# Optimization experiments

Hardware: AMD Instinct MI355X
Metric: run time of the kernel (lower is better)

The kernel has to match this reference:

```python
import jax, jax.numpy as jnp
import numpy as np
from jax import lax

WINDOW_SIZE = 11
SIGMA = 1.5
MAX_VAL = 1.0
C1 = (MAX_VAL * 0.01) ** 2
C2 = (MAX_VAL * 0.03) ** 2


def _make_window(channel: int, k: int = WINDOW_SIZE, sigma: float = SIGMA) -> np.ndarray:
    x = np.arange(k, dtype=np.float64)
    g = np.exp(-((x - k // 2) ** 2) / (2.0 * sigma ** 2))
    g = (g / g.sum()).astype(np.float32)
    # rank-1 separable 3D window, built as dense [C,1,k,k,k] kernel (OIDHW, groups=C)
    w3 = g[:, None, None] * g[None, :, None] * g[None, None, :]
    return np.broadcast_to(w3, (channel, 1, k, k, k)).copy()


def _dwconv3d(x, kernel, pad):
    # depthwise 3D conv, SAME padding for odd kernel
    return lax.conv_general_dilated(
        x, kernel, window_strides=(1, 1, 1), padding=[(pad, pad)] * 3,
        dimension_numbers=("NCDHW", "OIDHW", "NCDHW"),
        feature_group_count=kernel.shape[0])


def setup_inputs() -> dict:
    key = jax.random.key(0)
    k1, k2 = jax.random.split(key)
    shape = (2, 4, 64, 160, 160)  # [B, C, D, H, W]
    img1 = jax.random.uniform(k1, shape, dtype=jnp.float32)
    img2 = jax.random.uniform(k2, shape, dtype=jnp.float32)
    return {"img1": img1, "img2": img2}


def reference(img1, img2):
    channel = img1.shape[1]
    window = jnp.asarray(_make_window(channel))
    pad = WINDOW_SIZE // 2
    # mask = ones_like(img1) in the original -> identity multiply, omitted
    mu1 = _dwconv3d(img1, window, pad)
    mu2 = _dwconv3d(img2, window, pad)
    mu1_sq = mu1 * mu1
    mu2_sq = mu2 * mu2
    mu1_mu2 = mu1 * mu2
    sigma1_sq = _dwconv3d(img1 * img1, window, pad) - mu1_sq
    sigma2_sq = _dwconv3d(img2 * img2, window, pad) - mu2_sq
    sigma12 = _dwconv3d(img1 * img2, window, pad) - mu1_mu2
    ssim_map = ((2.0 * mu1_mu2 + C1) * (2.0 * sigma12 + C2)) / (
        (mu1_sq + mu2_sq + C1) * (sigma1_sq + sigma2_sq + C2))
    ssim = jnp.mean(ssim_map, axis=(0, 2, 3, 4))  # per-channel SSIM, shape [C]
    return 1.0 - ssim
```

## Files before the change

### kernel.cpp

```cpp
#include <hip/hip_runtime.h>
#include <math.h>

typedef float v2f __attribute__((ext_vector_type(2)));

namespace {

constexpr int C_DIM = 4;
constexpr int D_DIM = 64;
constexpr int H_DIM = 160;
constexpr int W_DIM = 160;

constexpr int TH = 20;
constexpr int TW = 20;
constexpr int HALO = 5;
constexpr int EH = 30;
constexpr int EW = 30;
constexpr int XST = 31;
constexpr int MST = 21;
constexpr int NPIX = EH * EW;

constexpr int TILES_W = 8;
constexpr int TPC = 64;
constexpr int D_SPLIT = 2;
constexpr int DCH = D_DIM / D_SPLIT;
constexpr int NBLOCKS = D_SPLIT * 2 * C_DIM * TPC;

constexpr float C1f = 1e-4f;
constexpr float C2f = 9e-4f;
constexpr float INV_N = 1.0f / (2.0f * 64.0f * 160.0f * 160.0f);

struct GW { float g[11]; };

}

__global__ void finalize_kernel(const float* __restrict__ partial,
                                float* __restrict__ out) {
    const int tid = threadIdx.x;
    const int c = tid >> 6;
    const int lane = tid & 63;
    float s = 0.0f;
#pragma unroll
    for (int r = 0; r < D_SPLIT * 2; ++r)
        s += partial[(r * C_DIM + c) * TPC + lane];
#pragma unroll
    for (int off = 32; off > 0; off >>= 1) s += __shfl_down(s, off, 64);
    if (lane == 0 && c < C_DIM) out[c] = 1.0f - s * INV_N;
}

__global__ __launch_bounds__(256, 2) void ssim3d_kernel(
    const float* __restrict__ img1, const float* __restrict__ img2,
    float* __restrict__ partial, GW gwp) {

    const int bid = blockIdx.x;
    const int tile = bid % TPC;
    const int c = (bid / TPC) % C_DIM;
    const int rest = bid / (TPC * C_DIM);
    const int b = rest & 1;
    const int dh = rest >> 1;
    const int h0 = (tile / TILES_W) * TH;
    const int w0 = (tile % TILES_W) * TW;

    const int d_lo = dh * DCH;
    const int s_base = (d_lo == 0) ? 0 : ((d_lo - HALO) & ~3);
    const int s_hi = min(D_DIM - 1, d_lo + DCH - 1 + HALO);
    const bool has_tail = (d_lo + DCH == D_DIM);

    const long planeHW = (long)H_DIM * W_DIM;
    const long volbase = (long)(b * C_DIM + c) * D_DIM * planeHW;
    const long org = volbase + (long)(h0 - HALO) * W_DIM + (w0 - HALO);
    const float* __restrict__ p1 = img1 + org;
    const float* __restrict__ p2 = img2 + org;

    const bool interior = (h0 >= HALO) && (h0 + TH + HALO <= H_DIM) &&
                          (w0 >= HALO) && (w0 + TW + HALO <= W_DIM);

    __shared__ v2f    xy[2][EH][XST];
    __shared__ float4 mid[2][EH][MST];
    __shared__ float  rbuf[4];

    const int tid = threadIdx.x;

    int hh_[4], ww_[4], off_[4];
    bool live_[4], ok_[4];
#pragma unroll
    for (int k = 0; k < 4; ++k) {
        const int e = tid + k * 256;
        live_[k] = (e < NPIX);
        const int hh = e / EW;
        const int ww = e - hh * EW;
        hh_[k] = hh; ww_[k] = ww;
        off_[k] = hh * W_DIM + ww;
        const int gh = h0 - HALO + hh;
        const int gw = w0 - HALO + ww;
        ok_[k] = ((unsigned)gh < (unsigned)H_DIM) &&
                 ((unsigned)gw < (unsigned)W_DIM);
    }

    auto fetch_slice = [&](int s, v2f lv[4]) {
        const long sb = (long)s * planeHW;
#pragma unroll
        for (int k = 0; k < 4; ++k) {
            lv[k] = (v2f){0.0f, 0.0f};
            if (live_[k] && (interior || ok_[k])) {
                const long gi = sb + off_[k];
                lv[k].x = p1[gi];
                lv[k].y = p2[gi];
            }
        }
    };
    auto commit_slice = [&](int buf, const v2f lv[4]) {
#pragma unroll
        for (int k = 0; k < 4; ++k)
            if (live_[k]) xy[buf][hh_[k]][ww_[k]] = lv[k];
    };

    const bool wactive = (tid < 150);
    const int whh = tid % 30;
    const int wg  = (tid / 30) * 4;

    auto wconv = [&](int cur) {
        v2f a0 = {0.f,0.f}, a1 = {0.f,0.f}, a2 = {0.f,0.f}, a3 = {0.f,0.f};
        v2f q0 = {0.f,0.f}, q1 = {0.f,0.f}, q2 = {0.f,0.f}, q3 = {0.f,0.f};
#pragma unroll
        for (int t = 0; t < 14; ++t) {
            const v2f xv = xy[cur][whh][wg + t];
            v2f qp;
            qp.x = fmaf(xv.x, xv.x, xv.y * xv.y);
            qp.y = xv.x * xv.y;
            if (t <= 10) {
                const v2f g2 = {gwp.g[t], gwp.g[t]};
                a0 = __builtin_elementwise_fma(g2, xv, a0);
                q0 = __builtin_elementwise_fma(g2, qp, q0);
            }
            if (t >= 1 && t <= 11) {
                const v2f g2 = {gwp.g[t-1], gwp.g[t-1]};
                a1 = __builtin_elementwise_fma(g2, xv, a1);
                q1 = __builtin_elementwise_fma(g2, qp, q1);
            }
            if (t >= 2 && t <= 12) {
                const v2f g2 = {gwp.g[t-2], gwp.g[t-2]};
                a2 = __builtin_elementwise_fma(g2, xv, a2);
                q2 = __builtin_elementwise_fma(g2, qp, q2);
            }
            if (t >= 3) {
                const v2f g2 = {gwp.g[t-3], gwp.g[t-3]};
                a3 = __builtin_elementwise_fma(g2, xv, a3);
                q3 = __builtin_elementwise_fma(g2, qp, q3);
            }
        }
        mid[cur][whh][wg]     = make_float4(a0.x, a0.y, q0.x, q0.y);
        mid[cur][whh][wg + 1] = make_float4(a1.x, a1.y, q1.x, q1.y);
        mid[cur][whh][wg + 2] = make_float4(a2.x, a2.y, q2.x, q2.y);
        mid[cur][whh][wg + 3] = make_float4(a3.x, a3.y, q3.x, q3.y);
    };

    const bool hworker = (tid < 200);
    const int hw = tid % 20;
    const int hb = (tid / 20) * 2;

    float accum = 0.0f;
    auto ssim_add = [&](v2f mxy, v2f mqp) {
        const float m1 = mxy.x, m2 = mxy.y;
        const float q = mqp.x, pp = mqp.y;
        const float m1s = m1 * m1;
        const float m2s = m2 * m2;
        const float m12 = m1 * m2;
        const float spp = q - m1s - m2s;
        const float s12 = pp - m12;
        const float num = (2.0f * m12 + C1f) * (2.0f * s12 + C2f);
        const float den = (m1s + m2s + C1f) * (spp + C2f);
        accum = fmaf(num, __builtin_amdgcn_rcpf(den), accum);
    };

    v2f w0xy[14], w0qp[14], w1xy[14], w1qp[14];
#pragma unroll
    for (int i = 0; i < 14; ++i) {
        w0xy[i] = (v2f){0.f, 0.f}; w0qp[i] = (v2f){0.f, 0.f};
        w1xy[i] = (v2f){0.f, 0.f}; w1qp[i] = (v2f){0.f, 0.f};
    }

    {
        v2f lv[4];
        fetch_slice(s_base, lv);
        commit_slice(0, lv);
    }
    __syncthreads();

    for (int sb = s_base; sb <= s_hi; sb += 4) {
#pragma unroll
        for (int u = 0; u < 4; ++u) {
            const int s = sb + u;
            if (s > s_hi) break;
            v2f lv[4];
            const bool have_next = (s + 1 <= s_hi);
            if (have_next) fetch_slice(s + 1, lv);
            if (wactive) wconv(u & 1);
            if (have_next) commit_slice((u + 1) & 1, lv);
            __syncthreads();
            if (hworker) {
                v2f z0x = {0.f,0.f}, z0q = {0.f,0.f};
                v2f z1x = {0.f,0.f}, z1q = {0.f,0.f};
#pragma unroll
                for (int t = 0; t < 12; ++t) {
                    const float4 m = mid[u & 1][hb + t][hw];
                    const v2f ma = {m.x, m.y};
                    const v2f mb = {m.z, m.w};
                    if (t <= 10) {
                        const v2f g2 = {gwp.g[t], gwp.g[t]};
                        z0x = __builtin_elementwise_fma(g2, ma, z0x);
                        z0q = __builtin_elementwise_fma(g2, mb, z0q);
                    }
                    if (t >= 1) {
                        const v2f g2 = {gwp.g[t-1], gwp.g[t-1]};
                        z1x = __builtin_elementwise_fma(g2, ma, z1x);
                        z1q = __builtin_elementwise_fma(g2, mb, z1q);
                    }
                }
                w0xy[10 + u] = z0x; w0qp[10 + u] = z0q;
                w1xy[10 + u] = z1x; w1qp[10 + u] = z1q;
                if (s >= d_lo + HALO) {
                    v2f mx0 = {0.f,0.f}, mq0 = {0.f,0.f};
                    v2f mx1 = {0.f,0.f}, mq1 = {0.f,0.f};
#pragma unroll
                    for (int t = 0; t < 11; ++t) {
                        const v2f g2 = {gwp.g[t], gwp.g[t]};
                        mx0 = __builtin_elementwise_fma(g2, w0xy[u + t], mx0);
                        mq0 = __builtin_elementwise_fma(g2, w0qp[u + t], mq0);
                        mx1 = __builtin_elementwise_fma(g2, w1xy[u + t], mx1);
                        mq1 = __builtin_elementwise_fma(g2, w1qp[u + t], mq1);
                    }
                    ssim_add(mx0, mq0);
                    ssim_add(mx1, mq1);
                }
            }
        }
        if (hworker) {
#pragma unroll
            for (int k = 0; k < 10; ++k) {
                w0xy[k] = w0xy[k + 4]; w0qp[k] = w0qp[k + 4];
                w1xy[k] = w1xy[k + 4]; w1qp[k] = w1qp[k + 4];
            }
        }
    }

    if (has_tail && hworker) {
#pragma unroll
        for (int i = 10; i < 14; ++i) {
            w0xy[i] = (v2f){0.f, 0.f}; w0qp[i] = (v2f){0.f, 0.f};
            w1xy[i] = (v2f){0.f, 0.f}; w1qp[i] = (v2f){0.f, 0.f};
        }
#pragma unroll
        for (int u2 = 0; u2 < 5; ++u2) {
            v2f mx0 = {0.f,0.f}, mq0 = {0.f,0.f};
            v2f mx1 = {0.f,0.f}, mq1 = {0.f,0.f};
#pragma unroll
            for (int t = 0; t < 11; ++t) {
                if (u2 + t <= 13) {
                    const v2f g2 = {gwp.g[t], gwp.g[t]};
                    mx0 = __builtin_elementwise_fma(g2, w0xy[u2 + t], mx0);
                    mq0 = __builtin_elementwise_fma(g2, w0qp[u2 + t], mq0);
                    mx1 = __builtin_elementwise_fma(g2, w1xy[u2 + t], mx1);
                    mq1 = __builtin_elementwise_fma(g2, w1qp[u2 + t], mq1);
                }
            }
            ssim_add(mx0, mq0);
            ssim_add(mx1, mq1);
        }
    }

#pragma unroll
    for (int off = 32; off > 0; off >>= 1) accum += __shfl_down(accum, off, 64);
    const int wave = tid >> 6;
    const int lane = tid & 63;
    if (lane == 0) rbuf[wave] = accum;
    __syncthreads();
    if (tid == 0) partial[bid] = rbuf[0] + rbuf[1] + rbuf[2] + rbuf[3];
}

extern "C" void kernel_launch(void* const* d_in, const int* in_sizes, int n_in,
                              void* d_out, int out_size, void* d_ws, size_t ws_size,
                              hipStream_t stream) {
    const float* img1 = (const float*)d_in[0];
    const float* img2 = (const float*)d_in[1];
    float* out = (float*)d_out;
    float* partial = (float*)d_ws;

    GW gw;
    {
        double gd[11];
        double ssum = 0.0;
        for (int i = 0; i < 11; ++i) {
            const double t = (double)(i - 5);
            gd[i] = exp(-(t * t) / 4.5);
            ssum += gd[i];
        }
        for (int i = 0; i < 11; ++i) gw.g[i] = (float)(gd[i] / ssum);
    }

    ssim3d_kernel<<<NBLOCKS, 256, 0, stream>>>(img1, img2, partial, gw);
    finalize_kernel<<<1, 256, 0, stream>>>(partial, out);
}
```

Before: 226.0 us.

## Shrink spatial tile to 16x16 with one output per thread and fewer registers

Changes the H/W tile from 20x20 to 16x16, giving 100 tiles per channel and more blocks overall. The H-pass now has all 256 threads each compute one output column, which removes the second register window set. The W-pass now produces 2 outputs per thread instead of 4. Launch bounds rise to 3 blocks per CU to use the freed registers. The cost is more halo overhead, since each 26x26 staged tile serves only 16x16 outputs, so there are more redundant global loads and conv work per output.

```diff
diff --git a/kernel.cpp b/kernel.cpp
--- a/kernel.cpp
+++ b/kernel.cpp
@@ -10,17 +10,17 @@
 constexpr int H_DIM = 160;
 constexpr int W_DIM = 160;
 
-constexpr int TH = 20;
-constexpr int TW = 20;
+constexpr int TH = 16;
+constexpr int TW = 16;
 constexpr int HALO = 5;
-constexpr int EH = 30;
-constexpr int EW = 30;
-constexpr int XST = 31;
-constexpr int MST = 21;
+constexpr int EH = 26;
+constexpr int EW = 26;
+constexpr int XST = 27;
+constexpr int MST = 17;
 constexpr int NPIX = EH * EW;
 
-constexpr int TILES_W = 8;
-constexpr int TPC = 64;
+constexpr int TILES_W = 10;
+constexpr int TPC = 100;
 constexpr int D_SPLIT = 2;
 constexpr int DCH = D_DIM / D_SPLIT;
 constexpr int NBLOCKS = D_SPLIT * 2 * C_DIM * TPC;
@@ -40,14 +40,17 @@
     const int lane = tid & 63;
     float s = 0.0f;
 #pragma unroll
-    for (int r = 0; r < D_SPLIT * 2; ++r)
-        s += partial[(r * C_DIM + c) * TPC + lane];
+    for (int r = 0; r < D_SPLIT * 2; ++r) {
+        const int base = (r * C_DIM + c) * TPC;
+        s += partial[base + lane];
+        if (lane < TPC - 64) s += partial[base + 64 + lane];
+    }
 #pragma unroll
     for (int off = 32; off > 0; off >>= 1) s += __shfl_down(s, off, 64);
     if (lane == 0 && c < C_DIM) out[c] = 1.0f - s * INV_N;
 }
 
-__global__ __launch_bounds__(256, 2) void ssim3d_kernel(
+__global__ __launch_bounds__(256, 3) void ssim3d_kernel(
     const float* __restrict__ img1, const float* __restrict__ img2,
     float* __restrict__ partial, GW gwp) {
 
@@ -80,50 +83,55 @@
 
     const int tid = threadIdx.x;
 
-    int hh_[4], ww_[4], off_[4];
-    bool live_[4], ok_[4];
-#pragma unroll
-    for (int k = 0; k < 4; ++k) {
+    int off_[3], loff_[3];
+    unsigned okmask = 0;
+#pragma unroll
+    for (int k = 0; k < 3; ++k) {
         const int e = tid + k * 256;
-        live_[k] = (e < NPIX);
         const int hh = e / EW;
         const int ww = e - hh * EW;
-        hh_[k] = hh; ww_[k] = ww;
         off_[k] = hh * W_DIM + ww;
+        loff_[k] = hh * XST + ww;
         const int gh = h0 - HALO + hh;
         const int gw = w0 - HALO + ww;
-        ok_[k] = ((unsigned)gh < (unsigned)H_DIM) &&
-                 ((unsigned)gw < (unsigned)W_DIM);
-    }
-
-    auto fetch_slice = [&](int s, v2f lv[4]) {
+        if (((unsigned)gh < (unsigned)H_DIM) &&
+            ((unsigned)gw < (unsigned)W_DIM))
+            okmask |= 1u << k;
+    }
+    const bool live2 = (tid < NPIX - 512);
+
+    auto fetch_slice = [&](int s, v2f lv[3]) {
         const long sb = (long)s * planeHW;
 #pragma unroll
-        for (int k = 0; k < 4; ++k) {
+        for (int k = 0; k < 3; ++k) {
             lv[k] = (v2f){0.0f, 0.0f};
-            if (live_[k] && (interior || ok_[k])) {
+            const bool live = (k < 2) || live2;
+            if (live && (interior || ((okmask >> k) & 1u))) {
                 const long gi = sb + off_[k];
                 lv[k].x = p1[gi];
                 lv[k].y = p2[gi];
             }
         }
     };
-    auto commit_slice = [&](int buf, const v2f lv[4]) {
-#pragma unroll
-        for (int k = 0; k < 4; ++k)
-            if (live_[k]) xy[buf][hh_[k]][ww_[k]] = lv[k];
-    };
-
-    const bool wactive = (tid < 150);
-    const int whh = tid % 30;
-    const int wg  = (tid / 30) * 4;
+    auto commit_slice = [&](int buf, const v2f lv[3]) {
+        v2f* base = &xy[buf][0][0];
+#pragma unroll
+        for (int k = 0; k < 3; ++k) {
+            const bool live = (k < 2) || live2;
+            if (live) base[loff_[k]] = lv[k];
+        }
+    };
+
+    const bool wactive = (tid < 208);
+    const int whh = tid % 26;
+    const int wg2 = (tid / 26) * 2;
 
     auto wconv = [&](int cur) {
-        v2f a0 = {0.f,0.f}, a1 = {0.f,0.f}, a2 = {0.f,0.f}, a3 = {0.f,0.f};
-        v2f q0 = {0.f,0.f}, q1 = {0.f,0.f}, q2 = {0.f,0.f}, q3 = {0.f,0.f};
-#pragma unroll
-        for (int t = 0; t < 14; ++t) {
-            const v2f xv = xy[cur][whh][wg + t];
+        v2f a0 = {0.f,0.f}, a1 = {0.f,0.f};
+        v2f q0 = {0.f,0.f}, q1 = {0.f,0.f};
+#pragma unroll
+        for (int t = 0; t < 12; ++t) {
+            const v2f xv = xy[cur][whh][wg2 + t];
             v2f qp;
             qp.x = fmaf(xv.x, xv.x, xv.y * xv.y);
             qp.y = xv.x * xv.y;
@@ -132,31 +140,18 @@
                 a0 = __builtin_elementwise_fma(g2, xv, a0);
                 q0 = __builtin_elementwise_fma(g2, qp, q0);
             }
-            if (t >= 1 && t <= 11) {
+            if (t >= 1) {
                 const v2f g2 = {gwp.g[t-1], gwp.g[t-1]};
                 a1 = __builtin_elementwise_fma(g2, xv, a1);
                 q1 = __builtin_elementwise_fma(g2, qp, q1);
             }
-            if (t >= 2 && t <= 12) {
-                const v2f g2 = {gwp.g[t-2], gwp.g[t-2]};
-                a2 = __builtin_elementwise_fma(g2, xv, a2);
-                q2 = __builtin_elementwise_fma(g2, qp, q2);
-            }
-            if (t >= 3) {
-                const v2f g2 = {gwp.g[t-3], gwp.g[t-3]};
-                a3 = __builtin_elementwise_fma(g2, xv, a3);
-                q3 = __builtin_elementwise_fma(g2, qp, q3);
-            }
-        }
-        mid[cur][whh][wg]     = make_float4(a0.x, a0.y, q0.x, q0.y);
-        mid[cur][whh][wg + 1] = make_float4(a1.x, a1.y, q1.x, q1.y);
-        mid[cur][whh][wg + 2] = make_float4(a2.x, a2.y, q2.x, q2.y);
-        mid[cur][whh][wg + 3] = make_float4(a3.x, a3.y, q3.x, q3.y);
-    };
-
-    const bool hworker = (tid < 200);
-    const int hw = tid % 20;
-    const int hb = (tid / 20) * 2;
+        }
+        mid[cur][whh][wg2]     = make_float4(a0.x, a0.y, q0.x, q0.y);
+        mid[cur][whh][wg2 + 1] = make_float4(a1.x, a1.y, q1.x, q1.y);
+    };
+
+    const int hw = tid & 15;
+    const int hy = tid >> 4;
 
     float accum = 0.0f;
     auto ssim_add = [&](v2f mxy, v2f mqp) {
@@ -172,15 +167,14 @@
         accum = fmaf(num, __builtin_amdgcn_rcpf(den), accum);
     };
 
-    v2f w0xy[14], w0qp[14], w1xy[14], w1qp[14];
+    v2f w0xy[14], w0qp[14];
 #pragma unroll
     for (int i = 0; i < 14; ++i) {
         w0xy[i] = (v2f){0.f, 0.f}; w0qp[i] = (v2f){0.f, 0.f};
-        w1xy[i] = (v2f){0.f, 0.f}; w1qp[i] = (v2f){0.f, 0.f};
     }
 
     {
-        v2f lv[4];
+        v2f lv[3];
         fetch_slice(s_base, lv);
         commit_slice(0, lv);
     }
@@ -191,80 +185,61 @@
         for (int u = 0; u < 4; ++u) {
             const int s = sb + u;
             if (s > s_hi) break;
-            v2f lv[4];
+            v2f lv[3];
             const bool have_next = (s + 1 <= s_hi);
             if (have_next) fetch_slice(s + 1, lv);
             if (wactive) wconv(u & 1);
             if (have_next) commit_slice((u + 1) & 1, lv);
             __syncthreads();
-            if (hworker) {
-                v2f z0x = {0.f,0.f}, z0q = {0.f,0.f};
-                v2f z1x = {0.f,0.f}, z1q = {0.f,0.f};
-#pragma unroll
-                for (int t = 0; t < 12; ++t) {
-                    const float4 m = mid[u & 1][hb + t][hw];
+            {
+                v2f zx = {0.f,0.f}, zq = {0.f,0.f};
+#pragma unroll
+                for (int t = 0; t < 11; ++t) {
+                    const float4 m = mid[u & 1][hy + t][hw];
                     const v2f ma = {m.x, m.y};
                     const v2f mb = {m.z, m.w};
-                    if (t <= 10) {
-                        const v2f g2 = {gwp.g[t], gwp.g[t]};
-                        z0x = __builtin_elementwise_fma(g2, ma, z0x);
-                        z0q = __builtin_elementwise_fma(g2, mb, z0q);
-                    }
-                    if (t >= 1) {
-                        const v2f g2 = {gwp.g[t-1], gwp.g[t-1]};
-                        z1x = __builtin_elementwise_fma(g2, ma, z1x);
-                        z1q = __builtin_elementwise_fma(g2, mb, z1q);
-                    }
+                    const v2f g2 = {gwp.g[t], gwp.g[t]};
+                    zx = __builtin_elementwise_fma(g2, ma, zx);
+                    zq = __builtin_elementwise_fma(g2, mb, zq);
                 }
-                w0xy[10 + u] = z0x; w0qp[10 + u] = z0q;
-                w1xy[10 + u] = z1x; w1qp[10 + u] = z1q;
+                w0xy[10 + u] = zx; w0qp[10 + u] = zq;
                 if (s >= d_lo + HALO) {
                     v2f mx0 = {0.f,0.f}, mq0 = {0.f,0.f};
-                    v2f mx1 = {0.f,0.f}, mq1 = {0.f,0.f};
 #pragma unroll
                     for (int t = 0; t < 11; ++t) {
                         const v2f g2 = {gwp.g[t], gwp.g[t]};
                         mx0 = __builtin_elementwise_fma(g2, w0xy[u + t], mx0);
                         mq0 = __builtin_elementwise_fma(g2, w0qp[u + t], mq0);
-                        mx1 = __builtin_elementwise_fma(g2, w1xy[u + t], mx1);
-                        mq1 = __builtin_elementwise_fma(g2, w1qp[u + t], mq1);
                     }
                     ssim_add(mx0, mq0);
-                    ssim_add(mx1, mq1);
                 }
             }
         }
-        if (hworker) {
+        {
 #pragma unroll
             for (int k = 0; k < 10; ++k) {
                 w0xy[k] = w0xy[k + 4]; w0qp[k] = w0qp[k + 4];
-                w1xy[k] = w1xy[k + 4]; w1qp[k] = w1qp[k + 4];
-            }
-        }
-    }
-
-    if (has_tail && hworker) {
+            }
+        }
+    }
+
+    if (has_tail) {
 #pragma unroll
         for (int i = 10; i < 14; ++i) {
             w0xy[i] = (v2f){0.f, 0.f}; w0qp[i] = (v2f){0.f, 0.f};
-            w1xy[i] = (v2f){0.f, 0.f}; w1qp[i] = (v2f){0.f, 0.f};
         }
 #pragma unroll
         for (int u2 = 0; u2 < 5; ++u2) {
             v2f mx0 = {0.f,0.f}, mq0 = {0.f,0.f};
-            v2f mx1 = {0.f,0.f}, mq1 = {0.f,0.f};
 #pragma unroll
             for (int t = 0; t < 11; ++t) {
                 if (u2 + t <= 13) {
                     const v2f g2 = {gwp.g[t], gwp.g[t]};
                     mx0 = __builtin_elementwise_fma(g2, w0xy[u2 + t], mx0);
                     mq0 = __builtin_elementwise_fma(g2, w0qp[u2 + t], mq0);
-                    mx1 = __builtin_elementwise_fma(g2, w1xy[u2 + t], mx1);
-                    mq1 = __builtin_elementwise_fma(g2, w1qp[u2 + t], mq1);
                 }
             }
             ssim_add(mx0, mq0);
-            ssim_add(mx1, mq1);
         }
     }
 
```

Result: no change. 221.6 us (-1.9%).
